# Kernel optimization log

Hardware: AMD Instinct MI355X
Metric: run time of the kernel (lower is better)

Reference implementation:

```python
import jax, jax.numpy as jnp
import numpy as np

EPS = 1e-08
SINKHORN_ITERS = 5
SINKHORN_TAU = 0.05


def l2_normalize(x, axis=-1):
    return x / (jnp.linalg.norm(x, axis=axis, keepdims=True) + EPS)


def sinkhorn_balanced(logits, iters=SINKHORN_ITERS, tau=SINKHORN_TAU):
    # logits: [B, N, K]
    b, n, k = logits.shape
    q = jnp.exp(logits / tau)
    q = q / (jnp.sum(q, axis=(1, 2), keepdims=True) + EPS)
    target_row = 1.0 / float(n)
    target_col = 1.0 / float(k)
    for _ in range(iters):
        q = q / (jnp.sum(q, axis=2, keepdims=True) + EPS) * target_row
        q = q / (jnp.sum(q, axis=1, keepdims=True) + EPS) * target_col
    q = q / (jnp.sum(q, axis=2, keepdims=True) + EPS)
    return q


def assign(x, proto):
    x_n = l2_normalize(x)          # [B,N,D]
    p_n = l2_normalize(proto)      # [K,D]
    sim = jnp.einsum('bnd,kd->bnk', x_n, p_n)
    a = sinkhorn_balanced(sim)
    z_rec = jnp.einsum('bnk,kd->bnd', a, p_n)
    return z_rec, a, sim


def setup_inputs() -> dict:
    key = jax.random.key(0)
    k1, k2, k3, k4 = jax.random.split(key, 4)
    B, N, D, K = 16, 1024, 256, 256
    return {
        'f_rgb': jax.random.normal(k1, (B, N, D), dtype=jnp.float32),
        'f_sn': jax.random.normal(k2, (B, N, D), dtype=jnp.float32),
        'proto_rgb': jax.random.normal(k3, (K, D), dtype=jnp.float32) * 0.02,
        'proto_sn': jax.random.normal(k4, (K, D), dtype=jnp.float32) * 0.02,
    }


def reference(f_rgb, f_sn, proto_rgb, proto_sn):
    z_rgb, assign_rgb, sim_rgb = assign(f_rgb, proto_rgb)
    z_sn, assign_sn, sim_sn = assign(f_sn, proto_sn)
    # cross-modal consistency maps: [B,N,N]
    rgb_to_sn = jnp.matmul(assign_rgb, jnp.swapaxes(assign_sn, -1, -2))
    sn_to_rgb = jnp.matmul(assign_sn, jnp.swapaxes(assign_rgb, -1, -2))
    sem_consistency = 0.5 * (
        1.0 - jnp.clip(jnp.mean(rgb_to_sn), 0.0, 1.0)
        + 1.0 - jnp.clip(jnp.mean(sn_to_rgb), 0.0, 1.0)
    )
    return (z_rgb, z_sn, assign_rgb, assign_sn, sim_rgb, sim_sn, sem_consistency)
```

## Files before the change

### kernel.cpp

```cpp
#include <hip/hip_runtime.h>
#include <hip/hip_bf16.h>
#include <cstdint>
#include <cstddef>

#define EPS 1e-8f

typedef __attribute__((ext_vector_type(8))) short short8;
typedef __attribute__((ext_vector_type(4))) float floatx4;

static constexpr int Bb = 16, Nn = 1024, Dd = 256, Kk = 256;
static constexpr int M = Bb * Nn;
static constexpr size_t PM = (size_t)M * 256;

static constexpr size_t OUT_Z      = 0;
static constexpr size_t OUT_ASSIGN = 2 * PM;
static constexpr size_t OUT_SIM    = 4 * PM;
static constexpr size_t OUT_SEM    = 6 * PM;

static constexpr size_t OFF_XN  = 0;
static constexpr size_t OFF_QB  = 16777216;
static constexpr size_t OFF_PN  = 33554432;
static constexpr size_t OFF_PNT = 33816576;
static constexpr size_t OFF_U   = 34078720;
static constexpr size_t OFF_T   = 34209792;
static constexpr size_t OFF_SC  = 34209920;
static constexpr size_t OFF_CS  = 34406528;
static constexpr size_t ZERO_OFF = OFF_T;
static constexpr size_t ZERO_SZ  = 128 + 196608 + 32768;
static constexpr int    NZ_FLOATS = (int)(ZERO_SZ / 4);

__device__ __forceinline__ unsigned short f2bf(float f) {
    unsigned int b = __float_as_uint(f);
    b += 0x7fffu + ((b >> 16) & 1u);
    return (unsigned short)(b >> 16);
}
__device__ __forceinline__ float bf2f(unsigned short u) {
    return __uint_as_float(((unsigned int)u) << 16);
}

typedef const __attribute__((address_space(1))) unsigned int* gas_u32p;
typedef __attribute__((address_space(3))) unsigned int* las_u32p;
__device__ __forceinline__ void lds_cp16(const unsigned short* g, short* l) {
    __builtin_amdgcn_global_load_lds((gas_u32p)g, (las_u32p)l, 16, 0, 0);
}

__global__ __launch_bounds__(256) void prep_kernel(const float* __restrict__ fr,
                                                   const float* __restrict__ fs,
                                                   unsigned short* __restrict__ xn) {
    int mod = blockIdx.y;
    int row = blockIdx.x * 4 + (threadIdx.x >> 6);
    int lane = threadIdx.x & 63;
    const float* src = (mod ? fs : fr) + (size_t)row * 256;
    float4 v = ((const float4*)src)[lane];
    float ss = v.x * v.x + v.y * v.y + v.z * v.z + v.w * v.w;
    #pragma unroll
    for (int m = 1; m < 64; m <<= 1) ss += __shfl_xor(ss, m);
    float sc = 1.0f / (sqrtf(ss) + EPS);
    ushort4 u4;
    u4.x = f2bf(v.x * sc); u4.y = f2bf(v.y * sc);
    u4.z = f2bf(v.z * sc); u4.w = f2bf(v.w * sc);
    *(ushort4*)(xn + (size_t)mod * PM + (size_t)row * 256 + lane * 4) = u4;
}

__global__ __launch_bounds__(64) void proto_kernel(const float* __restrict__ pr,
                                                   const float* __restrict__ ps,
                                                   unsigned short* __restrict__ pn,
                                                   unsigned short* __restrict__ pnt,
                                                   float* __restrict__ zp) {
    int gid = blockIdx.x * 64 + threadIdx.x;
    for (int i = gid; i < NZ_FLOATS; i += 32768) zp[i] = 0.f;

    int row = blockIdx.x & 255;
    int mod = blockIdx.x >> 8;
    const float* p = (mod ? ps : pr) + (size_t)row * 256;
    int lane = threadIdx.x;
    float4 v = ((const float4*)p)[lane];
    float ss = v.x * v.x + v.y * v.y + v.z * v.z + v.w * v.w;
    #pragma unroll
    for (int m = 1; m < 64; m <<= 1) ss += __shfl_xor(ss, m);
    float sc = 1.0f / (sqrtf(ss) + EPS);
    ushort4 u4;
    u4.x = f2bf(v.x * sc); u4.y = f2bf(v.y * sc);
    u4.z = f2bf(v.z * sc); u4.w = f2bf(v.w * sc);
    *(ushort4*)(pn + (size_t)mod * 65536 + (size_t)row * 256 + lane * 4) = u4;
    unsigned short* pt = pnt + (size_t)mod * 65536 + row;
    pt[(size_t)(lane * 4 + 0) * 256] = u4.x;
    pt[(size_t)(lane * 4 + 1) * 256] = u4.y;
    pt[(size_t)(lane * 4 + 2) * 256] = u4.z;
    pt[(size_t)(lane * 4 + 3) * 256] = u4.w;
}

template <int MODE>
__global__ __launch_bounds__(256) void gemm_kernel(const unsigned short* __restrict__ Asrc,
                                                   const unsigned short* __restrict__ Bsrc,
                                                   unsigned short* __restrict__ qb,
                                                   float* __restrict__ doutf,
                                                   float* __restrict__ Tg) {
    __shared__ short Al[8192];
    __shared__ short Bl[8192];

    int bx = blockIdx.x;
    int by = blockIdx.y;
    int mod = blockIdx.z;
    int t = threadIdx.x;
    int lane = t & 63, wv = t >> 6;
    int wrow = (wv >> 1) * 64, wcol = (wv & 1) * 64;
    int g = lane >> 4, ml = lane & 15;

    const unsigned short* A0 = Asrc + (size_t)mod * PM + (size_t)by * 128 * 256;
    const unsigned short* B0 = Bsrc + (size_t)mod * 65536 + (size_t)bx * 128 * 256;

    floatx4 acc[4][4];
    #pragma unroll
    for (int i = 0; i < 4; i++)
        #pragma unroll
        for (int j = 0; j < 4; j++) acc[i][j] = (floatx4){0.f, 0.f, 0.f, 0.f};

    for (int kh = 0; kh < 4; kh++) {
        #pragma unroll
        for (int i = 0; i < 4; i++) {
            int sI = i * 256 + t;
            int r = sI >> 3, cs = sI & 7;
            int cg = cs ^ (r & 7);
            size_t goff = (size_t)r * 256 + kh * 64 + cg * 8;
            lds_cp16(A0 + goff, &Al[sI * 8]);
            lds_cp16(B0 + goff, &Bl[sI * 8]);
        }
        __syncthreads();
        #pragma unroll
        for (int ks = 0; ks < 2; ks++) {
            short8 af[4], bfr[4];
            int c = ks * 4 + g;
            #pragma unroll
            for (int mt = 0; mt < 4; mt++) {
                int row = wrow + mt * 16 + ml;
                af[mt] = *(const short8*)&Al[row * 64 + (c ^ (row & 7)) * 8];
            }
            #pragma unroll
            for (int nt = 0; nt < 4; nt++) {
                int row = wcol + nt * 16 + ml;
                bfr[nt] = *(const short8*)&Bl[row * 64 + (c ^ (row & 7)) * 8];
            }
            #pragma unroll
            for (int mt = 0; mt < 4; mt++)
                #pragma unroll
                for (int nt = 0; nt < 4; nt++)
                    acc[mt][nt] = __builtin_amdgcn_mfma_f32_16x16x32_bf16(af[mt], bfr[nt], acc[mt][nt], 0, 0, 0);
        }
        __syncthreads();
    }

    int g4 = g << 2;
    float tsum = 0.f;
    #pragma unroll
    for (int mt = 0; mt < 4; mt++)
        #pragma unroll
        for (int nt = 0; nt < 4; nt++)
            #pragma unroll
            for (int reg = 0; reg < 4; reg++) {
                float s = acc[mt][nt][reg];
                int row = by * 128 + wrow + mt * 16 + g4 + reg;
                int col = bx * 128 + wcol + nt * 16 + ml;
                size_t idx = (size_t)row * 256 + col;
                if (MODE == 0) {
                    doutf[OUT_SIM + (size_t)mod * PM + idx] = s;
                    unsigned short eb = f2bf(__expf(s * 20.0f));
                    qb[(size_t)mod * PM + idx] = eb;
                    tsum += bf2f(eb);
                } else {
                    doutf[OUT_Z + (size_t)mod * PM + idx] = s;
                }
            }
    if (MODE == 0) {
        #pragma unroll
        for (int mk = 1; mk < 64; mk <<= 1) tsum += __shfl_xor(tsum, mk);
        if (lane == 0) atomicAdd(&Tg[mod * 16 + (by >> 3)], tsum);
    }
}

__global__ __launch_bounds__(256) void pass_kernel(const unsigned short* __restrict__ qbg,
                                                   float* __restrict__ u,
                                                   const float* __restrict__ Tg,
                                                   float* __restrict__ Sc,
                                                   float* __restrict__ cs,
                                                   float* __restrict__ doutf,
                                                   unsigned short* __restrict__ abf,
                                                   int pass) {
    __shared__ float vcur[256];
    __shared__ float unl[32];
    __shared__ float wsum[4][256];
    int tile = blockIdx.x, b = blockIdx.y, mod = blockIdx.z;
    int t = threadIdx.x;
    {
        float v = 1.0f;
        for (int j = 1; j < pass; j++) {
            float sc = Sc[((size_t)(mod * 6 + j) * 16 + b) * 256 + t];
            v = v * (1.0f / 256.0f) / (v * sc + EPS);
        }
        vcur[t] = v;
    }
    __syncthreads();

    int r = t >> 3, q = t & 7;
    size_t row = (size_t)b * 1024 + tile * 32 + r;
    const unsigned short* qrow = qbg + ((size_t)mod * M + row) * 256;
    const short8* q8 = (const short8*)(qrow + q * 32);
    const float4* v4 = (const float4*)(vcur + q * 32);
    float sr = 0.f;
    #pragma unroll
    for (int i = 0; i < 4; i++) {
        short8 qv = q8[i];
        float4 va = v4[2 * i], vb = v4[2 * i + 1];
        sr += bf2f((unsigned short)qv[0]) * va.x + bf2f((unsigned short)qv[1]) * va.y
            + bf2f((unsigned short)qv[2]) * va.z + bf2f((unsigned short)qv[3]) * va.w
            + bf2f((unsigned short)qv[4]) * vb.x + bf2f((unsigned short)qv[5]) * vb.y
            + bf2f((unsigned short)qv[6]) * vb.z + bf2f((unsigned short)qv[7]) * vb.w;
    }
    sr += __shfl_xor(sr, 1);
    sr += __shfl_xor(sr, 2);
    sr += __shfl_xor(sr, 4);

    float up = (pass == 1) ? 1.0f / (Tg[mod * 16 + b] + EPS) : u[(size_t)mod * M + row];
    float un;
    if (pass <= 5) un = up * (1.0f / 1024.0f) / (up * sr + EPS);
    else           un = up / (up * sr + EPS);
    if (q == 0) {
        if (pass <= 5) u[(size_t)mod * M + row] = un;
        unl[r] = un;
    }
    __syncthreads();

    int wv = t >> 6, lane = t & 63;
    float c0 = 0.f, c1 = 0.f, c2 = 0.f, c3 = 0.f;
    float4 vv = *(const float4*)(vcur + lane * 4);
    size_t rowbase = (size_t)mod * M + (size_t)b * 1024 + tile * 32;
    if (pass <= 5) {
        #pragma unroll
        for (int rr8 = 0; rr8 < 8; rr8++) {
            int rr = wv * 8 + rr8;
            float unr = unl[rr];
            ushort4 qv = *(const ushort4*)(qbg + (rowbase + rr) * 256 + lane * 4);
            c0 += bf2f(qv.x) * unr;
            c1 += bf2f(qv.y) * unr;
            c2 += bf2f(qv.z) * unr;
            c3 += bf2f(qv.w) * unr;
        }
    } else {
        float* aout = doutf + OUT_ASSIGN + (size_t)mod * PM;
        unsigned short* ab = abf + (size_t)mod * PM;
        #pragma unroll
        for (int rr8 = 0; rr8 < 8; rr8++) {
            int rr = wv * 8 + rr8;
            float unr = unl[rr];
            size_t ro = ((size_t)b * 1024 + tile * 32 + rr) * 256;
            ushort4 qv = *(const ushort4*)(qbg + (rowbase + rr) * 256 + lane * 4);
            float4 a = make_float4(bf2f(qv.x) * unr * vv.x, bf2f(qv.y) * unr * vv.y,
                                   bf2f(qv.z) * unr * vv.z, bf2f(qv.w) * unr * vv.w);
            *(float4*)(aout + ro + lane * 4) = a;
            ushort4 o;
            o.x = f2bf(a.x); o.y = f2bf(a.y); o.z = f2bf(a.z); o.w = f2bf(a.w);
            *(ushort4*)(ab + ro + lane * 4) = o;
            c0 += a.x; c1 += a.y; c2 += a.z; c3 += a.w;
        }
    }
    *(float4*)&wsum[wv][lane * 4] = make_float4(c0, c1, c2, c3);
    __syncthreads();
    {
        float ssum = wsum[0][t] + wsum[1][t] + wsum[2][t] + wsum[3][t];
        float* dst = (pass <= 5) ? &Sc[((size_t)(mod * 6 + pass) * 16 + b) * 256 + t]
                                 : &cs[((size_t)mod * 16 + b) * 256 + t];
        atomicAdd(dst, ssum);
    }
}

__global__ __launch_bounds__(256) void sem_kernel(const float* __restrict__ cs,
                                                  float* __restrict__ doutf) {
    int t = threadIdx.x;
    float s = 0.f;
    #pragma unroll
    for (int b = 0; b < 16; b++)
        s += cs[b * 256 + t] * cs[4096 + b * 256 + t];
    #pragma unroll
    for (int mk = 1; mk < 64; mk <<= 1) s += __shfl_xor(s, mk);
    __shared__ float red[4];
    if ((t & 63) == 0) red[t >> 6] = s;
    __syncthreads();
    if (t == 0) {
        float tot = red[0] + red[1] + red[2] + red[3];
        float mv = tot / 16777216.0f;
        mv = fminf(fmaxf(mv, 0.f), 1.f);
        doutf[OUT_SEM] = 1.0f - mv;
    }
}

extern "C" void kernel_launch(void* const* d_in, const int* in_sizes, int n_in,
                              void* d_out, int out_size, void* d_ws, size_t ws_size,
                              hipStream_t stream) {
    const float* f_rgb = (const float*)d_in[0];
    const float* f_sn  = (const float*)d_in[1];
    const float* p_rgb = (const float*)d_in[2];
    const float* p_sn  = (const float*)d_in[3];
    char* ws = (char*)d_ws;
    unsigned short* xn   = (unsigned short*)(ws + OFF_XN);
    unsigned short* abf  = (unsigned short*)(ws + OFF_XN);
    unsigned short* qb   = (unsigned short*)(ws + OFF_QB);
    unsigned short* pn   = (unsigned short*)(ws + OFF_PN);
    unsigned short* pnt  = (unsigned short*)(ws + OFF_PNT);
    float* u             = (float*)(ws + OFF_U);
    float* Tg            = (float*)(ws + OFF_T);
    float* Sc            = (float*)(ws + OFF_SC);
    float* cs            = (float*)(ws + OFF_CS);
    float* doutf         = (float*)d_out;

    proto_kernel<<<dim3(512), 64, 0, stream>>>(p_rgb, p_sn, pn, pnt, (float*)(ws + ZERO_OFF));
    prep_kernel<<<dim3(4096, 2), 256, 0, stream>>>(f_rgb, f_sn, xn);
    gemm_kernel<0><<<dim3(2, 128, 2), 256, 0, stream>>>(xn, pn, qb, doutf, Tg);
    for (int p = 1; p <= 6; p++)
        pass_kernel<<<dim3(32, 16, 2), 256, 0, stream>>>(qb, u, Tg, Sc, cs, doutf, abf, p);
    gemm_kernel<1><<<dim3(2, 128, 2), 256, 0, stream>>>(abf, pnt, qb, doutf, Tg);
    sem_kernel<<<1, 256, 0, stream>>>(cs, doutf);
}
```

Measured before the change: 208.4 us.

## Fuse Sinkhorn passes into one cooperative kernel keeping Q tile in LDS

Replaces six separate pass_kernel launches with a single cooperative kernel. Each block loads its 64x256 bf16 tile of Q into LDS once and reuses it across all six row/column normalization passes. Grid-wide syncs replace kernel boundaries, and column sums still go through global atomics. This avoids re-reading Q from global memory each pass and the per-launch overhead, at the cost of grid-sync latency and needing all 512 blocks co-resident (a fallback path keeps the old launches).

```diff
diff --git a/kernel.cpp b/kernel.cpp
--- a/kernel.cpp
+++ b/kernel.cpp
@@ -1,7 +1,10 @@
 #include <hip/hip_runtime.h>
 #include <hip/hip_bf16.h>
+#include <hip/hip_cooperative_groups.h>
 #include <cstdint>
 #include <cstddef>
+
+namespace cg = cooperative_groups;
 
 #define EPS 1e-8f
 
@@ -37,6 +40,7 @@
 __device__ __forceinline__ float bf2f(unsigned short u) {
     return __uint_as_float(((unsigned int)u) << 16);
 }
+__device__ __forceinline__ int VP(int c) { return c + ((c >> 5) << 2); }
 
 typedef const __attribute__((address_space(1))) unsigned int* gas_u32p;
 typedef __attribute__((address_space(3))) unsigned int* las_u32p;
@@ -175,6 +179,119 @@
         #pragma unroll
         for (int mk = 1; mk < 64; mk <<= 1) tsum += __shfl_xor(tsum, mk);
         if (lane == 0) atomicAdd(&Tg[mod * 16 + (by >> 3)], tsum);
+    }
+}
+
+__global__ __launch_bounds__(256, 2) void sinkhorn_fused(const unsigned short* __restrict__ qbg,
+                                                         const float* __restrict__ Tg,
+                                                         float* __restrict__ Sc,
+                                                         float* __restrict__ cs,
+                                                         float* __restrict__ doutf,
+                                                         unsigned short* __restrict__ abf) {
+    __shared__ unsigned short qt[64 * 264];
+    __shared__ float vpad[288];
+    __shared__ float unl[64];
+    __shared__ float wsum[4][256];
+
+    cg::grid_group gg = cg::this_grid();
+
+    int tile = blockIdx.x, b = blockIdx.y, mod = blockIdx.z;
+    int t = threadIdx.x;
+    int wv = t >> 6, lane = t & 63;
+    int r0 = t >> 3, qq = t & 7;
+
+    size_t rowg0 = (size_t)b * 1024 + tile * 64;
+    const unsigned short* qsrc = qbg + (size_t)mod * PM + rowg0 * 256;
+
+    #pragma unroll
+    for (int i = 0; i < 8; i++) {
+        int c = i * 256 + t;
+        int row = c >> 5, cc = c & 31;
+        *(short8*)&qt[row * 264 + cc * 8] = *(const short8*)(qsrc + (size_t)row * 256 + cc * 8);
+    }
+    float u0 = 1.0f / (Tg[mod * 16 + b] + EPS);
+
+    for (int pass = 1; pass <= 6; pass++) {
+        if (pass == 1) {
+            vpad[VP(t)] = 1.0f;
+        } else {
+            float scp = __hip_atomic_load(&Sc[((size_t)(mod * 6 + pass - 1) * 16 + b) * 256 + t],
+                                          __ATOMIC_RELAXED, __HIP_MEMORY_SCOPE_AGENT);
+            float v = vpad[VP(t)];
+            vpad[VP(t)] = v * (1.0f / 256.0f) / (v * scp + EPS);
+        }
+        __syncthreads();
+
+        const float* vb0 = &vpad[VP(qq * 32)];
+        #pragma unroll
+        for (int h = 0; h < 2; h++) {
+            int rr = r0 + h * 32;
+            const unsigned short* qrow = &qt[rr * 264 + qq * 32];
+            float sr = 0.f;
+            #pragma unroll
+            for (int i = 0; i < 4; i++) {
+                short8 qv = *(const short8*)(qrow + i * 8);
+                float4 va = *(const float4*)(vb0 + i * 8);
+                float4 vb = *(const float4*)(vb0 + i * 8 + 4);
+                sr += bf2f((unsigned short)qv[0]) * va.x + bf2f((unsigned short)qv[1]) * va.y
+                    + bf2f((unsigned short)qv[2]) * va.z + bf2f((unsigned short)qv[3]) * va.w
+                    + bf2f((unsigned short)qv[4]) * vb.x + bf2f((unsigned short)qv[5]) * vb.y
+                    + bf2f((unsigned short)qv[6]) * vb.z + bf2f((unsigned short)qv[7]) * vb.w;
+            }
+            sr += __shfl_xor(sr, 1);
+            sr += __shfl_xor(sr, 2);
+            sr += __shfl_xor(sr, 4);
+            float up = (pass == 1) ? u0 : unl[rr];
+            float un;
+            if (pass <= 5) un = up * (1.0f / 1024.0f) / (up * sr + EPS);
+            else           un = up / (up * sr + EPS);
+            if (qq == 0) unl[rr] = un;
+        }
+
+        float c0 = 0.f, c1 = 0.f, c2 = 0.f, c3 = 0.f;
+        if (pass <= 5) {
+            #pragma unroll
+            for (int h = 0; h < 2; h++)
+                #pragma unroll
+                for (int k = 0; k < 8; k++) {
+                    int rr = h * 32 + wv * 8 + k;
+                    float unr = unl[rr];
+                    ushort4 qv = *(const ushort4*)(&qt[rr * 264 + lane * 4]);
+                    c0 += bf2f(qv.x) * unr;
+                    c1 += bf2f(qv.y) * unr;
+                    c2 += bf2f(qv.z) * unr;
+                    c3 += bf2f(qv.w) * unr;
+                }
+        } else {
+            float4 vv = *(const float4*)(&vpad[VP(lane * 4)]);
+            float* aout = doutf + OUT_ASSIGN + (size_t)mod * PM;
+            unsigned short* ab = abf + (size_t)mod * PM;
+            #pragma unroll
+            for (int h = 0; h < 2; h++)
+                #pragma unroll
+                for (int k = 0; k < 8; k++) {
+                    int rr = h * 32 + wv * 8 + k;
+                    float unr = unl[rr];
+                    ushort4 qv = *(const ushort4*)(&qt[rr * 264 + lane * 4]);
+                    float4 a = make_float4(bf2f(qv.x) * unr * vv.x, bf2f(qv.y) * unr * vv.y,
+                                           bf2f(qv.z) * unr * vv.z, bf2f(qv.w) * unr * vv.w);
+                    size_t ro = (rowg0 + rr) * 256;
+                    *(float4*)(aout + ro + lane * 4) = a;
+                    ushort4 o;
+                    o.x = f2bf(a.x); o.y = f2bf(a.y); o.z = f2bf(a.z); o.w = f2bf(a.w);
+                    *(ushort4*)(ab + ro + lane * 4) = o;
+                    c0 += a.x; c1 += a.y; c2 += a.z; c3 += a.w;
+                }
+        }
+        *(float4*)&wsum[wv][lane * 4] = make_float4(c0, c1, c2, c3);
+        __syncthreads();
+        float ssum = wsum[0][t] + wsum[1][t] + wsum[2][t] + wsum[3][t];
+        if (pass <= 5) {
+            atomicAdd(&Sc[((size_t)(mod * 6 + pass) * 16 + b) * 256 + t], ssum);
+            gg.sync();
+        } else {
+            atomicAdd(&cs[((size_t)mod * 16 + b) * 256 + t], ssum);
+        }
     }
 }
 
@@ -315,8 +432,17 @@
     proto_kernel<<<dim3(512), 64, 0, stream>>>(p_rgb, p_sn, pn, pnt, (float*)(ws + ZERO_OFF));
     prep_kernel<<<dim3(4096, 2), 256, 0, stream>>>(f_rgb, f_sn, xn);
     gemm_kernel<0><<<dim3(2, 128, 2), 256, 0, stream>>>(xn, pn, qb, doutf, Tg);
-    for (int p = 1; p <= 6; p++)
-        pass_kernel<<<dim3(32, 16, 2), 256, 0, stream>>>(qb, u, Tg, Sc, cs, doutf, abf, p);
+
+    const unsigned short* qbc = qb;
+    const float* Tgc = Tg;
+    void* args[] = {(void*)&qbc, (void*)&Tgc, (void*)&Sc, (void*)&cs, (void*)&doutf, (void*)&abf};
+    hipError_t ce = hipLaunchCooperativeKernel(reinterpret_cast<void*>(sinkhorn_fused),
+                                               dim3(16, 16, 2), dim3(256), args, 0, stream);
+    if (ce != hipSuccess) {
+        for (int p = 1; p <= 6; p++)
+            pass_kernel<<<dim3(32, 16, 2), 256, 0, stream>>>(qb, u, Tg, Sc, cs, doutf, abf, p);
+    }
+
     gemm_kernel<1><<<dim3(2, 128, 2), 256, 0, stream>>>(abf, pnt, qb, doutf, Tg);
     sem_kernel<<<1, 256, 0, stream>>>(cs, doutf);
 }
```

Measured after the change: 475.9 us. 2.28x slower.

## Fuse input normalization into first GEMM and final Sinkhorn pass into second GEMM

Applied to the files above, without the earlier changes.

Removes the separate prep kernel: each first-GEMM block now loads fp32 feature rows, L2-normalizes them, and writes the whole 128x256 bf16 A tile into a swizzled 64KB LDS buffer. The sixth Sinkhorn pass is folded into the second GEMM, which recomputes v from the column sums, finishes the row normalization, writes the assignment output and builds its bf16 A tile in LDS. This removes the round-trip of the normalized features and the bf16 assignment copy through global memory, plus two launches. In exchange, both GEMM blocks normalize the same rows redundantly (two column blocks each), and the 80KB of LDS per block reduces occupancy.

```diff
diff --git a/kernel.cpp b/kernel.cpp
--- a/kernel.cpp
+++ b/kernel.cpp
@@ -17,7 +17,6 @@
 static constexpr size_t OUT_SIM    = 4 * PM;
 static constexpr size_t OUT_SEM    = 6 * PM;
 
-static constexpr size_t OFF_XN  = 0;
 static constexpr size_t OFF_QB  = 16777216;
 static constexpr size_t OFF_PN  = 33554432;
 static constexpr size_t OFF_PNT = 33816576;
@@ -42,24 +41,6 @@
 typedef __attribute__((address_space(3))) unsigned int* las_u32p;
 __device__ __forceinline__ void lds_cp16(const unsigned short* g, short* l) {
     __builtin_amdgcn_global_load_lds((gas_u32p)g, (las_u32p)l, 16, 0, 0);
-}
-
-__global__ __launch_bounds__(256) void prep_kernel(const float* __restrict__ fr,
-                                                   const float* __restrict__ fs,
-                                                   unsigned short* __restrict__ xn) {
-    int mod = blockIdx.y;
-    int row = blockIdx.x * 4 + (threadIdx.x >> 6);
-    int lane = threadIdx.x & 63;
-    const float* src = (mod ? fs : fr) + (size_t)row * 256;
-    float4 v = ((const float4*)src)[lane];
-    float ss = v.x * v.x + v.y * v.y + v.z * v.z + v.w * v.w;
-    #pragma unroll
-    for (int m = 1; m < 64; m <<= 1) ss += __shfl_xor(ss, m);
-    float sc = 1.0f / (sqrtf(ss) + EPS);
-    ushort4 u4;
-    u4.x = f2bf(v.x * sc); u4.y = f2bf(v.y * sc);
-    u4.z = f2bf(v.z * sc); u4.w = f2bf(v.w * sc);
-    *(ushort4*)(xn + (size_t)mod * PM + (size_t)row * 256 + lane * 4) = u4;
 }
 
 __global__ __launch_bounds__(64) void proto_kernel(const float* __restrict__ pr,
@@ -90,25 +71,45 @@
     pt[(size_t)(lane * 4 + 3) * 256] = u4.w;
 }
 
-template <int MODE>
-__global__ __launch_bounds__(256) void gemm_kernel(const unsigned short* __restrict__ Asrc,
-                                                   const unsigned short* __restrict__ Bsrc,
+__global__ __launch_bounds__(256) void gemm0_fused(const float* __restrict__ fr,
+                                                   const float* __restrict__ fs,
+                                                   const unsigned short* __restrict__ pn,
                                                    unsigned short* __restrict__ qb,
                                                    float* __restrict__ doutf,
                                                    float* __restrict__ Tg) {
-    __shared__ short Al[8192];
-    __shared__ short Bl[8192];
-
-    int bx = blockIdx.x;
-    int by = blockIdx.y;
-    int mod = blockIdx.z;
-    int t = threadIdx.x;
-    int lane = t & 63, wv = t >> 6;
+    __shared__ __align__(16) char smem[81920];
+    short* Afull = (short*)smem;
+    short* Bl    = (short*)(smem + 65536);
+
+    int bx = blockIdx.x, by = blockIdx.y, mod = blockIdx.z;
+    int t = threadIdx.x, lane = t & 63, wv = t >> 6;
     int wrow = (wv >> 1) * 64, wcol = (wv & 1) * 64;
     int g = lane >> 4, ml = lane & 15;
 
-    const unsigned short* A0 = Asrc + (size_t)mod * PM + (size_t)by * 128 * 256;
-    const unsigned short* B0 = Bsrc + (size_t)mod * 65536 + (size_t)bx * 128 * 256;
+    const float* F0 = (mod ? fs : fr) + (size_t)by * 128 * 256;
+    const unsigned short* B0 = pn + (size_t)mod * 65536 + (size_t)bx * 128 * 256;
+
+    for (int bs = 0; bs < 4; bs++) {
+        int rbase = wv * 32 + bs * 8;
+        float4 vv[8];
+        #pragma unroll
+        for (int i = 0; i < 8; i++)
+            vv[i] = ((const float4*)(F0 + (size_t)(rbase + i) * 256))[lane];
+        #pragma unroll
+        for (int i = 0; i < 8; i++) {
+            float ss = vv[i].x * vv[i].x + vv[i].y * vv[i].y
+                     + vv[i].z * vv[i].z + vv[i].w * vv[i].w;
+            #pragma unroll
+            for (int m = 1; m < 64; m <<= 1) ss += __shfl_xor(ss, m);
+            float sc = 1.0f / (sqrtf(ss) + EPS);
+            ushort4 u4;
+            u4.x = f2bf(vv[i].x * sc); u4.y = f2bf(vv[i].y * sc);
+            u4.z = f2bf(vv[i].z * sc); u4.w = f2bf(vv[i].w * sc);
+            int row = rbase + i;
+            int off = row * 256 + (((lane >> 1) ^ (row & 7)) << 3) + ((lane & 1) << 2);
+            *(ushort4*)&Afull[off] = u4;
+        }
+    }
 
     floatx4 acc[4][4];
     #pragma unroll
@@ -123,7 +124,6 @@
             int r = sI >> 3, cs = sI & 7;
             int cg = cs ^ (r & 7);
             size_t goff = (size_t)r * 256 + kh * 64 + cg * 8;
-            lds_cp16(A0 + goff, &Al[sI * 8]);
             lds_cp16(B0 + goff, &Bl[sI * 8]);
         }
         __syncthreads();
@@ -131,15 +131,16 @@
         for (int ks = 0; ks < 2; ks++) {
             short8 af[4], bfr[4];
             int c = ks * 4 + g;
+            int c8 = kh * 8 + c;
             #pragma unroll
             for (int mt = 0; mt < 4; mt++) {
                 int row = wrow + mt * 16 + ml;
-                af[mt] = *(const short8*)&Al[row * 64 + (c ^ (row & 7)) * 8];
+                af[mt] = *(const short8*)&Afull[row * 256 + ((c8 ^ (row & 7)) << 3)];
             }
             #pragma unroll
             for (int nt = 0; nt < 4; nt++) {
-                int row = wcol + nt * 16 + ml;
-                bfr[nt] = *(const short8*)&Bl[row * 64 + (c ^ (row & 7)) * 8];
+                int col = wcol + nt * 16 + ml;
+                bfr[nt] = *(const short8*)&Bl[col * 64 + ((c ^ (col & 7)) << 3)];
             }
             #pragma unroll
             for (int mt = 0; mt < 4; mt++)
@@ -162,29 +163,23 @@
                 int row = by * 128 + wrow + mt * 16 + g4 + reg;
                 int col = bx * 128 + wcol + nt * 16 + ml;
                 size_t idx = (size_t)row * 256 + col;
-                if (MODE == 0) {
-                    doutf[OUT_SIM + (size_t)mod * PM + idx] = s;
-                    unsigned short eb = f2bf(__expf(s * 20.0f));
-                    qb[(size_t)mod * PM + idx] = eb;
-                    tsum += bf2f(eb);
-                } else {
-                    doutf[OUT_Z + (size_t)mod * PM + idx] = s;
-                }
-            }
-    if (MODE == 0) {
-        #pragma unroll
-        for (int mk = 1; mk < 64; mk <<= 1) tsum += __shfl_xor(tsum, mk);
-        if (lane == 0) atomicAdd(&Tg[mod * 16 + (by >> 3)], tsum);
-    }
+                doutf[OUT_SIM + (size_t)mod * PM + idx] = s;
+                unsigned short eb = f2bf(__expf(s * 20.0f));
+                qb[(size_t)mod * PM + idx] = eb;
+                tsum += bf2f(eb);
+            }
+    #pragma unroll
+    for (int mk = 1; mk < 64; mk <<= 1) tsum += __shfl_xor(tsum, mk);
+    float* tred = (float*)(smem + 65536);
+    if (lane == 0) tred[wv] = tsum;
+    __syncthreads();
+    if (t == 0) atomicAdd(&Tg[mod * 16 + (by >> 3)], tred[0] + tred[1] + tred[2] + tred[3]);
 }
 
 __global__ __launch_bounds__(256) void pass_kernel(const unsigned short* __restrict__ qbg,
                                                    float* __restrict__ u,
                                                    const float* __restrict__ Tg,
                                                    float* __restrict__ Sc,
-                                                   float* __restrict__ cs,
-                                                   float* __restrict__ doutf,
-                                                   unsigned short* __restrict__ abf,
                                                    int pass) {
     __shared__ float vcur[256];
     __shared__ float unl[32];
@@ -221,56 +216,174 @@
     sr += __shfl_xor(sr, 4);
 
     float up = (pass == 1) ? 1.0f / (Tg[mod * 16 + b] + EPS) : u[(size_t)mod * M + row];
-    float un;
-    if (pass <= 5) un = up * (1.0f / 1024.0f) / (up * sr + EPS);
-    else           un = up / (up * sr + EPS);
+    float un = up * (1.0f / 1024.0f) / (up * sr + EPS);
     if (q == 0) {
-        if (pass <= 5) u[(size_t)mod * M + row] = un;
+        u[(size_t)mod * M + row] = un;
         unl[r] = un;
     }
     __syncthreads();
 
     int wv = t >> 6, lane = t & 63;
     float c0 = 0.f, c1 = 0.f, c2 = 0.f, c3 = 0.f;
-    float4 vv = *(const float4*)(vcur + lane * 4);
     size_t rowbase = (size_t)mod * M + (size_t)b * 1024 + tile * 32;
-    if (pass <= 5) {
-        #pragma unroll
-        for (int rr8 = 0; rr8 < 8; rr8++) {
-            int rr = wv * 8 + rr8;
-            float unr = unl[rr];
-            ushort4 qv = *(const ushort4*)(qbg + (rowbase + rr) * 256 + lane * 4);
-            c0 += bf2f(qv.x) * unr;
-            c1 += bf2f(qv.y) * unr;
-            c2 += bf2f(qv.z) * unr;
-            c3 += bf2f(qv.w) * unr;
-        }
-    } else {
-        float* aout = doutf + OUT_ASSIGN + (size_t)mod * PM;
-        unsigned short* ab = abf + (size_t)mod * PM;
-        #pragma unroll
-        for (int rr8 = 0; rr8 < 8; rr8++) {
-            int rr = wv * 8 + rr8;
-            float unr = unl[rr];
-            size_t ro = ((size_t)b * 1024 + tile * 32 + rr) * 256;
-            ushort4 qv = *(const ushort4*)(qbg + (rowbase + rr) * 256 + lane * 4);
-            float4 a = make_float4(bf2f(qv.x) * unr * vv.x, bf2f(qv.y) * unr * vv.y,
-                                   bf2f(qv.z) * unr * vv.z, bf2f(qv.w) * unr * vv.w);
-            *(float4*)(aout + ro + lane * 4) = a;
-            ushort4 o;
-            o.x = f2bf(a.x); o.y = f2bf(a.y); o.z = f2bf(a.z); o.w = f2bf(a.w);
-            *(ushort4*)(ab + ro + lane * 4) = o;
-            c0 += a.x; c1 += a.y; c2 += a.z; c3 += a.w;
-        }
+    #pragma unroll
+    for (int rr8 = 0; rr8 < 8; rr8++) {
+        int rr = wv * 8 + rr8;
+        float unr = unl[rr];
+        ushort4 qv = *(const ushort4*)(qbg + (rowbase + rr) * 256 + lane * 4);
+        c0 += bf2f(qv.x) * unr;
+        c1 += bf2f(qv.y) * unr;
+        c2 += bf2f(qv.z) * unr;
+        c3 += bf2f(qv.w) * unr;
     }
     *(float4*)&wsum[wv][lane * 4] = make_float4(c0, c1, c2, c3);
     __syncthreads();
     {
         float ssum = wsum[0][t] + wsum[1][t] + wsum[2][t] + wsum[3][t];
-        float* dst = (pass <= 5) ? &Sc[((size_t)(mod * 6 + pass) * 16 + b) * 256 + t]
-                                 : &cs[((size_t)mod * 16 + b) * 256 + t];
-        atomicAdd(dst, ssum);
-    }
+        atomicAdd(&Sc[((size_t)(mod * 6 + pass) * 16 + b) * 256 + t], ssum);
+    }
+}
+
+__global__ __launch_bounds__(256) void gemm1_fused(const unsigned short* __restrict__ qbg,
+                                                   const unsigned short* __restrict__ pnt,
+                                                   const float* __restrict__ u,
+                                                   const float* __restrict__ Sc,
+                                                   float* __restrict__ cs,
+                                                   float* __restrict__ doutf) {
+    __shared__ __align__(16) char smem[81920];
+    short* Afull = (short*)smem;
+    short* Bl    = (short*)(smem + 65536);
+    float* vl    = (float*)(smem + 65536);
+    float* unl   = (float*)(smem + 65536 + 1024);
+    float* wsum  = (float*)(smem + 65536 + 2048);
+
+    int bx = blockIdx.x, by = blockIdx.y, mod = blockIdx.z;
+    int b = by >> 3;
+    int t = threadIdx.x, lane = t & 63, wv = t >> 6;
+    int wrow = (wv >> 1) * 64, wcol = (wv & 1) * 64;
+    int g = lane >> 4, ml = lane & 15;
+    int r = t >> 3, q = t & 7;
+    size_t rowg0 = (size_t)by * 128;
+
+    if (t < 256) {
+        float v = 1.0f;
+        #pragma unroll
+        for (int j = 1; j <= 5; j++) {
+            float scv = Sc[((size_t)(mod * 6 + j) * 16 + b) * 256 + t];
+            v = v * (1.0f / 256.0f) / (v * scv + EPS);
+        }
+        vl[t] = v;
+    }
+    __syncthreads();
+
+    const float* vb0 = vl + q * 32;
+    for (int s = 0; s < 4; s++) {
+        int rl = s * 32 + r;
+        size_t rowg = rowg0 + rl;
+        const short8* q8 = (const short8*)(qbg + ((size_t)mod * PM + rowg * 256) + q * 32);
+        float sr = 0.f;
+        #pragma unroll
+        for (int i = 0; i < 4; i++) {
+            short8 qv = q8[i];
+            float4 va = *(const float4*)(vb0 + i * 8);
+            float4 vb = *(const float4*)(vb0 + i * 8 + 4);
+            sr += bf2f((unsigned short)qv[0]) * va.x + bf2f((unsigned short)qv[1]) * va.y
+                + bf2f((unsigned short)qv[2]) * va.z + bf2f((unsigned short)qv[3]) * va.w
+                + bf2f((unsigned short)qv[4]) * vb.x + bf2f((unsigned short)qv[5]) * vb.y
+                + bf2f((unsigned short)qv[6]) * vb.z + bf2f((unsigned short)qv[7]) * vb.w;
+        }
+        sr += __shfl_xor(sr, 1);
+        sr += __shfl_xor(sr, 2);
+        sr += __shfl_xor(sr, 4);
+        float up = u[(size_t)mod * M + rowg];
+        float un = up / (up * sr + EPS);
+        if (q == 0) unl[rl] = un;
+    }
+    __syncthreads();
+
+    {
+        float c0 = 0.f, c1 = 0.f, c2 = 0.f, c3 = 0.f;
+        float4 vv = *(const float4*)(vl + lane * 4);
+        float* aout = doutf + OUT_ASSIGN + (size_t)mod * PM;
+        for (int s = 0; s < 4; s++) {
+            #pragma unroll
+            for (int k = 0; k < 8; k++) {
+                int rl = s * 32 + wv * 8 + k;
+                size_t rowg = rowg0 + rl;
+                float unr = unl[rl];
+                ushort4 qv = *(const ushort4*)(qbg + ((size_t)mod * PM + rowg * 256) + lane * 4);
+                float4 a = make_float4(bf2f(qv.x) * unr * vv.x, bf2f(qv.y) * unr * vv.y,
+                                       bf2f(qv.z) * unr * vv.z, bf2f(qv.w) * unr * vv.w);
+                if (bx == 0) *(float4*)(aout + rowg * 256 + lane * 4) = a;
+                ushort4 o;
+                o.x = f2bf(a.x); o.y = f2bf(a.y); o.z = f2bf(a.z); o.w = f2bf(a.w);
+                int off = rl * 256 + (((lane >> 1) ^ (rl & 7)) << 3) + ((lane & 1) << 2);
+                *(ushort4*)&Afull[off] = o;
+                c0 += a.x; c1 += a.y; c2 += a.z; c3 += a.w;
+            }
+        }
+        *(float4*)&wsum[wv * 256 + lane * 4] = make_float4(c0, c1, c2, c3);
+    }
+    __syncthreads();
+    if (bx == 0 && t < 256) {
+        float ssum = wsum[0 * 256 + t] + wsum[1 * 256 + t] + wsum[2 * 256 + t] + wsum[3 * 256 + t];
+        atomicAdd(&cs[((size_t)mod * 16 + b) * 256 + t], ssum);
+    }
+    __syncthreads();
+
+    const unsigned short* B0 = pnt + (size_t)mod * 65536 + (size_t)bx * 128 * 256;
+    floatx4 acc[4][4];
+    #pragma unroll
+    for (int i = 0; i < 4; i++)
+        #pragma unroll
+        for (int j = 0; j < 4; j++) acc[i][j] = (floatx4){0.f, 0.f, 0.f, 0.f};
+
+    for (int kh = 0; kh < 4; kh++) {
+        #pragma unroll
+        for (int i = 0; i < 4; i++) {
+            int sI = i * 256 + t;
+            int rr = sI >> 3, cc = sI & 7;
+            int cg = cc ^ (rr & 7);
+            size_t goff = (size_t)rr * 256 + kh * 64 + cg * 8;
+            lds_cp16(B0 + goff, &Bl[sI * 8]);
+        }
+        __syncthreads();
+        #pragma unroll
+        for (int ks = 0; ks < 2; ks++) {
+            short8 af[4], bfr[4];
+            int c = ks * 4 + g;
+            int c8 = kh * 8 + c;
+            #pragma unroll
+            for (int mt = 0; mt < 4; mt++) {
+                int row = wrow + mt * 16 + ml;
+                af[mt] = *(const short8*)&Afull[row * 256 + ((c8 ^ (row & 7)) << 3)];
+            }
+            #pragma unroll
+            for (int nt = 0; nt < 4; nt++) {
+                int col = wcol + nt * 16 + ml;
+                bfr[nt] = *(const short8*)&Bl[col * 64 + ((c ^ (col & 7)) << 3)];
+            }
+            #pragma unroll
+            for (int mt = 0; mt < 4; mt++)
+                #pragma unroll
+                for (int nt = 0; nt < 4; nt++)
+                    acc[mt][nt] = __builtin_amdgcn_mfma_f32_16x16x32_bf16(af[mt], bfr[nt], acc[mt][nt], 0, 0, 0);
+        }
+        __syncthreads();
+    }
+
+    int g4 = g << 2;
+    float* dst = doutf + OUT_Z + (size_t)mod * PM;
+    #pragma unroll
+    for (int mt = 0; mt < 4; mt++)
+        #pragma unroll
+        for (int nt = 0; nt < 4; nt++)
+            #pragma unroll
+            for (int reg = 0; reg < 4; reg++) {
+                int row = by * 128 + wrow + mt * 16 + g4 + reg;
+                int col = bx * 128 + wcol + nt * 16 + ml;
+                dst[(size_t)row * 256 + col] = acc[mt][nt][reg];
+            }
 }
 
 __global__ __launch_bounds__(256) void sem_kernel(const float* __restrict__ cs,
@@ -301,8 +414,6 @@
     const float* p_rgb = (const float*)d_in[2];
     const float* p_sn  = (const float*)d_in[3];
     char* ws = (char*)d_ws;
-    unsigned short* xn   = (unsigned short*)(ws + OFF_XN);
-    unsigned short* abf  = (unsigned short*)(ws + OFF_XN);
     unsigned short* qb   = (unsigned short*)(ws + OFF_QB);
     unsigned short* pn   = (unsigned short*)(ws + OFF_PN);
     unsigned short* pnt  = (unsigned short*)(ws + OFF_PNT);
@@ -313,10 +424,9 @@
     float* doutf         = (float*)d_out;
 
     proto_kernel<<<dim3(512), 64, 0, stream>>>(p_rgb, p_sn, pn, pnt, (float*)(ws + ZERO_OFF));
-    prep_kernel<<<dim3(4096, 2), 256, 0, stream>>>(f_rgb, f_sn, xn);
-    gemm_kernel<0><<<dim3(2, 128, 2), 256, 0, stream>>>(xn, pn, qb, doutf, Tg);
-    for (int p = 1; p <= 6; p++)
-        pass_kernel<<<dim3(32, 16, 2), 256, 0, stream>>>(qb, u, Tg, Sc, cs, doutf, abf, p);
-    gemm_kernel<1><<<dim3(2, 128, 2), 256, 0, stream>>>(abf, pnt, qb, doutf, Tg);
+    gemm0_fused<<<dim3(2, 128, 2), 256, 0, stream>>>(f_rgb, f_sn, pn, qb, doutf, Tg);
+    for (int p = 1; p <= 5; p++)
+        pass_kernel<<<dim3(32, 16, 2), 256, 0, stream>>>(qb, u, Tg, Sc, p);
+    gemm1_fused<<<dim3(2, 128, 2), 256, 0, stream>>>(qb, pnt, u, Sc, cs, doutf);
     sem_kernel<<<1, 256, 0, stream>>>(cs, doutf);
 }
```

Measured after the change: 192.1 us. 7.8% less time.
